# Kernel tuning notes

Measured on AMD Instinct MI355X. Metric: run time of the kernel, lower is better.

## Reference

```python
import jax, jax.numpy as jnp
import numpy as np


def setup_inputs() -> dict:
    key = jax.random.key(0)
    k1, k2, k3, k4 = jax.random.split(key, 4)
    B, T, E, H = 16, 2048, 1024, 128
    x = jax.random.normal(k1, (B, T, E), dtype=jnp.float32)
    Wk = jax.random.normal(k2, (E, H), dtype=jnp.float32) * (E ** -0.5)
    Wq = jax.random.normal(k3, (E, H), dtype=jnp.float32) * (E ** -0.5)
    Wv = jax.random.normal(k4, (E, H), dtype=jnp.float32) * (E ** -0.5)
    return {"x": x, "Wk": Wk, "Wq": Wq, "Wv": Wv}


def reference(x, Wk, Wq, Wv):
    # x: [B,T,E]; Wk/Wq/Wv: [E,H]
    B, T, E = x.shape
    H = Wk.shape[1]
    k = jnp.einsum('bte,eh->bth', x, Wk)
    q = jnp.einsum('bte,eh->bth', x, Wq)
    v = jnp.einsum('bte,eh->bth', x, Wv)
    # scores [B,T,T]; original masks with -inf THEN scales (equivalent math)
    scores = jnp.einsum('bqh,bkh->bqk', q, k) * (H ** -0.5)
    causal = jnp.tril(jnp.ones((T, T), dtype=bool))
    scores = jnp.where(causal, scores, -jnp.inf)
    weights = jax.nn.softmax(scores, axis=-1)
    # dropout disabled (eval mode reference)
    return jnp.einsum('bqk,bkh->bqh', weights, v)
```

## Files before the change

### kernel.cpp

```cpp
#include <hip/hip_runtime.h>

#define B_ 16
#define T_ 2048
#define E_ 1024
#define H_ 128

typedef short bf16x8 __attribute__((ext_vector_type(8)));
typedef float f32x4 __attribute__((ext_vector_type(4)));
typedef unsigned short u16x4 __attribute__((ext_vector_type(4)));

static __device__ __forceinline__ unsigned short f2bf(float f) {
    unsigned int u = __float_as_uint(f);
    u += 0x7FFFu + ((u >> 16) & 1u);
    return (unsigned short)(u >> 16);
}
static __device__ __forceinline__ unsigned int pk2(unsigned short a, unsigned short b) {
    return (unsigned int)a | ((unsigned int)b << 16);
}
static __device__ __forceinline__ bf16x8 frag(uint4 v) {
    return __builtin_bit_cast(bf16x8, v);
}
static __device__ __forceinline__ void gl16(const unsigned short* g, unsigned short* l) {
    __builtin_amdgcn_global_load_lds(
        (const __attribute__((address_space(1))) void*)g,
        (__attribute__((address_space(3))) void*)l, 16, 0, 0);
}

__global__ __launch_bounds__(256) void cvtw_kernel(
    const float* __restrict__ w0, const float* __restrict__ w1,
    const float* __restrict__ w2, unsigned short* __restrict__ wt)
{
    int g   = blockIdx.x * 256 + threadIdx.x;
    int arr = g >> 14;
    int rem = g & 16383;
    int h   = rem >> 7;
    int e0  = (rem & 127) * 8;
    const float* src = (arr == 0) ? w0 : (arr == 1) ? w1 : w2;
    unsigned short b[8];
#pragma unroll
    for (int i = 0; i < 8; i++) b[i] = f2bf(src[(size_t)(e0 + i) * H_ + h]);
    uint4 o;
    o.x = pk2(b[0], b[1]); o.y = pk2(b[2], b[3]);
    o.z = pk2(b[4], b[5]); o.w = pk2(b[6], b[7]);
    *(uint4*)&wt[(size_t)(arr * 128 + h) * E_ + e0] = o;
}

__global__ __launch_bounds__(512, 4) void proj_kernel(
    const float* __restrict__ x,
    const unsigned short* __restrict__ wt,
    unsigned short* __restrict__ q_ws,
    unsigned short* __restrict__ kp_ws,
    unsigned short* __restrict__ vt_ws)
{
    const int m0 = blockIdx.x * 64;
    __shared__ __align__(16) unsigned short As[2][64 * 32];
    __shared__ __align__(16) unsigned short Bs[2][384 * 32];

    const int tid  = threadIdx.x;
    const int lane = tid & 63;
    const int w    = tid >> 6;
    const int quad = lane >> 4;
    const int lm   = lane & 15;
    const int wc   = w * 48;

    const int arow = tid >> 3;
    const int acol = (tid & 7) * 4;
    const float* gx = x + (size_t)(m0 + arow) * E_ + acol;

    const int brow = tid >> 2;
    const int bcol = (tid & 3) * 8;
    const unsigned short* gw = wt + (size_t)brow * E_ + bcol;

    const f32x4 z4 = {0.f, 0.f, 0.f, 0.f};
    f32x4 acc[4][3];
#pragma unroll
    for (int i = 0; i < 4; i++)
#pragma unroll
        for (int j = 0; j < 3; j++) acc[i][j] = z4;

    auto stageB = [&](int kb, int buf) {
        const unsigned short* g = gw + kb * 32;
        unsigned short* l = &Bs[buf][tid * 8];
        gl16(g,                    l);
        gl16(g + (size_t)128 * E_, l + 4096);
        gl16(g + (size_t)256 * E_, l + 8192);
    };
    auto writeA = [&](float4 v, int buf) {
        u16x4 o;
        o[0] = f2bf(v.x); o[1] = f2bf(v.y);
        o[2] = f2bf(v.z); o[3] = f2bf(v.w);
        *(u16x4*)&As[buf][arow * 32 + acol] = o;
    };

    float4 a = *(const float4*)gx;
    stageB(0, 0);
    writeA(a, 0);
    a = *(const float4*)(gx + 32);

    for (int kb = 0; kb < 32; kb++) {
        const int cb = kb & 1;
        __syncthreads();

        const int kb2 = (kb + 2 < 32) ? kb + 2 : 31;
        float4 n = *(const float4*)(gx + kb2 * 32);
        if (kb + 1 < 32) {
            stageB(kb + 1, cb ^ 1);
            writeA(a, cb ^ 1);
        }

        bf16x8 af[4], bf[3];
#pragma unroll
        for (int am = 0; am < 4; am++)
            af[am] = frag(*(const uint4*)&As[cb][(am * 16 + lm) * 32 + quad * 8]);
#pragma unroll
        for (int bn = 0; bn < 3; bn++)
            bf[bn] = frag(*(const uint4*)&Bs[cb][(wc + bn * 16 + lm) * 32 + quad * 8]);
#pragma unroll
        for (int am = 0; am < 4; am++)
#pragma unroll
            for (int bn = 0; bn < 3; bn++)
                acc[am][bn] = __builtin_amdgcn_mfma_f32_16x16x32_bf16(
                    af[am], bf[bn], acc[am][bn], 0, 0, 0);

        a = n;
    }

#pragma unroll
    for (int am = 0; am < 4; am++)
#pragma unroll
        for (int bn = 0; bn < 3; bn++) {
            const int gcol  = wc + bn * 16 + lm;
            const int sel   = gcol >> 7;
            const int c     = gcol & 127;
            const int rbase = m0 + am * 16 + quad * 4;
            const int bb    = rbase >> 11;
            const int t     = rbase & 2047;
            if (sel == 0) {
#pragma unroll
                for (int r = 0; r < 4; r++)
                    q_ws[(size_t)(rbase + r) * H_ + c] = f2bf(acc[am][bn][r]);
            } else if (sel == 1) {
#pragma unroll
                for (int r = 0; r < 4; r++) {
                    int tt = t + r;
                    kp_ws[(size_t)(bb * 64 + (tt >> 5)) * 4096 +
                          (c >> 5) * 1024 + (tt & 31) * 32 + (c & 31)] =
                        f2bf(acc[am][bn][r]);
                }
            } else {
                u16x4 pv;
#pragma unroll
                for (int r = 0; r < 4; r++) pv[r] = f2bf(acc[am][bn][r]);
                *(u16x4*)&vt_ws[((size_t)(bb * 64 + (t >> 5)) * 128 + c) * 32 + (t & 31)] = pv;
            }
        }
}

__global__ __launch_bounds__(256, 2) void attn_kernel(
    const unsigned short* __restrict__ q_ws,
    const unsigned short* __restrict__ kp_ws,
    const unsigned short* __restrict__ vt_ws,
    float* __restrict__ out)
{
    __shared__ __align__(16) unsigned short Ks[3][4096];
    __shared__ __align__(16) unsigned short Vs[3][4096];
    __shared__ __align__(16) unsigned short Ps[4][16][40];

    const int bid   = blockIdx.x;
    const int batch = bid & 15;
    const int p     = (bid >> 4) & 15;
    const int tau   = (bid >> 8) ? (31 - p) : p;
    const int nkt   = 2 * tau + 2;

    const int tid  = threadIdx.x;
    const int lane = tid & 63;
    const int ww   = tid >> 6;
    const int quad = lane >> 4;
    const int lm   = lane & 15;
    const float scale = 0.08838834764831845f;

    bf16x8 ones;
#pragma unroll
    for (int i = 0; i < 8; i++) ones[i] = (short)0x3F80;
    const f32x4 z4 = {0.f, 0.f, 0.f, 0.f};

    const size_t bq = (size_t)batch * T_ * H_;
    const int so = ww * 1024 + lane * 8;
    const unsigned short* Kt = kp_ws + (size_t)(batch * 64) * 4096 + so;
    const unsigned short* Vt = vt_ws + (size_t)(batch * 64) * 4096 + so;

    auto stage = [&](int t, int b) {
        const unsigned short* kg = Kt + (size_t)t * 4096;
        const unsigned short* vg = Vt + (size_t)t * 4096;
        gl16(kg,       &Ks[b][ww * 1024]);
        gl16(kg + 512, &Ks[b][ww * 1024 + 512]);
        gl16(vg,       &Vs[b][ww * 1024]);
        gl16(vg + 512, &Vs[b][ww * 1024 + 512]);
    };

    bf16x8 qf[4];
#pragma unroll
    for (int h = 0; h < 4; h++)
        qf[h] = frag(*(const uint4*)(q_ws + bq +
                 (size_t)(tau * 64 + ww * 16 + lm) * H_ + h * 32 + quad * 8));

    f32x4 o[9];
#pragma unroll
    for (int f = 0; f < 9; f++) o[f] = z4;

    stage(0, 0);
    stage(1, 1);

    for (int kt = 0; kt < nkt; kt++) {
        const int cb = kt % 3;
        asm volatile("s_waitcnt vmcnt(4) lgkmcnt(0)" ::: "memory");
        __builtin_amdgcn_sched_barrier(0);
        __builtin_amdgcn_s_barrier();
        __builtin_amdgcn_sched_barrier(0);

        int ks = kt + 2; if (ks > nkt - 1) ks = nkt - 1;
        stage(ks, (kt + 2) % 3);

        f32x4 st0 = z4, st1 = z4;
        __builtin_amdgcn_s_setprio(1);
#pragma unroll
        for (int h = 0; h < 4; h++) {
            bf16x8 kf0 = frag(*(const uint4*)&Ks[cb][(h * 32 + lm) * 32 + quad * 8]);
            bf16x8 kf1 = frag(*(const uint4*)&Ks[cb][(h * 32 + 16 + lm) * 32 + quad * 8]);
            st0 = __builtin_amdgcn_mfma_f32_16x16x32_bf16(kf0, qf[h], st0, 0, 0, 0);
            st1 = __builtin_amdgcn_mfma_f32_16x16x32_bf16(kf1, qf[h], st1, 0, 0, 0);
        }
        __builtin_amdgcn_s_setprio(0);

        const int qg = tau * 64 + ww * 16 + lm;
        const int k0 = kt * 32;
        u16x4 pa, pb;
#pragma unroll
        for (int r = 0; r < 4; r++) {
            int kv0 = k0 + quad * 4 + r;
            float e0 = __expf(st0[r] * scale);
            float e1 = __expf(st1[r] * scale);
            pa[r] = (kv0      <= qg) ? f2bf(e0) : (unsigned short)0;
            pb[r] = (kv0 + 16 <= qg) ? f2bf(e1) : (unsigned short)0;
        }
        *(u16x4*)&Ps[ww][lm][quad * 4]      = pa;
        *(u16x4*)&Ps[ww][lm][16 + quad * 4] = pb;
        bf16x8 pf = frag(*(const uint4*)&Ps[ww][lm][quad * 8]);

        __builtin_amdgcn_s_setprio(1);
#pragma unroll
        for (int f = 0; f < 8; f++) {
            bf16x8 vfr = frag(*(const uint4*)&Vs[cb][(f * 16 + lm) * 32 + quad * 8]);
            o[f] = __builtin_amdgcn_mfma_f32_16x16x32_bf16(pf, vfr, o[f], 0, 0, 0);
        }
        o[8] = __builtin_amdgcn_mfma_f32_16x16x32_bf16(pf, ones, o[8], 0, 0, 0);
        __builtin_amdgcn_s_setprio(0);
    }

    float* op = out + bq + (size_t)(tau * 64 + ww * 16) * H_;
#pragma unroll
    for (int r = 0; r < 4; r++) {
        float inv = 1.f / o[8][r];
#pragma unroll
        for (int f = 0; f < 8; f++)
            op[(size_t)(quad * 4 + r) * H_ + f * 16 + lm] = o[f][r] * inv;
    }
}

extern "C" void kernel_launch(void* const* d_in, const int* in_sizes, int n_in,
                              void* d_out, int out_size, void* d_ws, size_t ws_size,
                              hipStream_t stream)
{
    const float* x  = (const float*)d_in[0];
    const float* Wk = (const float*)d_in[1];
    const float* Wq = (const float*)d_in[2];
    const float* Wv = (const float*)d_in[3];
    float* out = (float*)d_out;

    const size_t MH = (size_t)B_ * T_ * H_;
    unsigned short* q_ws  = (unsigned short*)d_ws;
    unsigned short* kp_ws = q_ws + MH;
    unsigned short* vt_ws = kp_ws + MH;
    unsigned short* wt    = vt_ws + MH;

    cvtw_kernel<<<dim3(192), dim3(256), 0, stream>>>(Wq, Wk, Wv, wt);
    proj_kernel<<<dim3(512), dim3(512), 0, stream>>>(x, wt, q_ws, kp_ws, vt_ws);
    attn_kernel<<<dim3(512), dim3(256), 0, stream>>>(q_ws, kp_ws, vt_ws, out);
}
```

Before: 283.7 us.

## Retile projection GEMM to 128x128 blocks with a grid split over Q/K/V

```diff
diff --git a/kernel.cpp b/kernel.cpp
--- a/kernel.cpp
+++ b/kernel.cpp
@@ -45,113 +45,125 @@
     *(uint4*)&wt[(size_t)(arr * 128 + h) * E_ + e0] = o;
 }
 
-__global__ __launch_bounds__(512, 4) void proj_kernel(
+__global__ __launch_bounds__(256, 3) void proj_kernel(
     const float* __restrict__ x,
     const unsigned short* __restrict__ wt,
     unsigned short* __restrict__ q_ws,
     unsigned short* __restrict__ kp_ws,
     unsigned short* __restrict__ vt_ws)
 {
-    const int m0 = blockIdx.x * 64;
-    __shared__ __align__(16) unsigned short As[2][64 * 32];
-    __shared__ __align__(16) unsigned short Bs[2][384 * 32];
+    const int m0 = blockIdx.x * 128;
+    const int by = blockIdx.y;
+    __shared__ __align__(16) unsigned short As[2][128 * 32];
+    __shared__ __align__(16) unsigned short Bs[2][128 * 32];
 
     const int tid  = threadIdx.x;
     const int lane = tid & 63;
     const int w    = tid >> 6;
     const int quad = lane >> 4;
     const int lm   = lane & 15;
-    const int wc   = w * 48;
-
-    const int arow = tid >> 3;
-    const int acol = (tid & 7) * 4;
-    const float* gx = x + (size_t)(m0 + arow) * E_ + acol;
-
-    const int brow = tid >> 2;
-    const int bcol = (tid & 3) * 8;
-    const unsigned short* gw = wt + (size_t)brow * E_ + bcol;
+    const int rw   = (w & 1) * 64;
+    const int cw   = (w >> 1) * 64;
+
+    const int srow = w * 32 + (lane >> 2);
+    const int sch  = (lane & 3) * 8;
+    const unsigned short* gb0 = wt + (size_t)(by * 128 + srow) * E_ + sch;
+    const unsigned short* gb1 = gb0 + (size_t)16 * E_;
+
+    const int arow = tid >> 1;
+    const int acs  = (tid & 1) * 16;
+    const float* gxa = x + (size_t)(m0 + arow) * E_ + acs;
 
     const f32x4 z4 = {0.f, 0.f, 0.f, 0.f};
-    f32x4 acc[4][3];
+    f32x4 acc[4][4];
 #pragma unroll
     for (int i = 0; i < 4; i++)
 #pragma unroll
-        for (int j = 0; j < 3; j++) acc[i][j] = z4;
+        for (int j = 0; j < 4; j++) acc[i][j] = z4;
 
     auto stageB = [&](int kb, int buf) {
-        const unsigned short* g = gw + kb * 32;
-        unsigned short* l = &Bs[buf][tid * 8];
-        gl16(g,                    l);
-        gl16(g + (size_t)128 * E_, l + 4096);
-        gl16(g + (size_t)256 * E_, l + 8192);
+        gl16(gb0 + kb * 32, &Bs[buf][w * 1024]);
+        gl16(gb1 + kb * 32, &Bs[buf][w * 1024 + 512]);
     };
-    auto writeA = [&](float4 v, int buf) {
-        u16x4 o;
-        o[0] = f2bf(v.x); o[1] = f2bf(v.y);
-        o[2] = f2bf(v.z); o[3] = f2bf(v.w);
-        *(u16x4*)&As[buf][arow * 32 + acol] = o;
+    float4 av0, av1, av2, av3;
+    auto ldA = [&](int kb) {
+        const float* g = gxa + kb * 32;
+        av0 = *(const float4*)g;
+        av1 = *(const float4*)(g + 4);
+        av2 = *(const float4*)(g + 8);
+        av3 = *(const float4*)(g + 12);
     };
-
-    float4 a = *(const float4*)gx;
+    auto writeA = [&](int buf) {
+        uint4 o0, o1;
+        o0.x = pk2(f2bf(av0.x), f2bf(av0.y));
+        o0.y = pk2(f2bf(av0.z), f2bf(av0.w));
+        o0.z = pk2(f2bf(av1.x), f2bf(av1.y));
+        o0.w = pk2(f2bf(av1.z), f2bf(av1.w));
+        o1.x = pk2(f2bf(av2.x), f2bf(av2.y));
+        o1.y = pk2(f2bf(av2.z), f2bf(av2.w));
+        o1.z = pk2(f2bf(av3.x), f2bf(av3.y));
+        o1.w = pk2(f2bf(av3.z), f2bf(av3.w));
+        *(uint4*)&As[buf][arow * 32 + acs]     = o0;
+        *(uint4*)&As[buf][arow * 32 + acs + 8] = o1;
+    };
+
+    ldA(0);
     stageB(0, 0);
-    writeA(a, 0);
-    a = *(const float4*)(gx + 32);
+    writeA(0);
+    ldA(1);
 
     for (int kb = 0; kb < 32; kb++) {
         const int cb = kb & 1;
         __syncthreads();
 
-        const int kb2 = (kb + 2 < 32) ? kb + 2 : 31;
-        float4 n = *(const float4*)(gx + kb2 * 32);
         if (kb + 1 < 32) {
             stageB(kb + 1, cb ^ 1);
-            writeA(a, cb ^ 1);
-        }
-
-        bf16x8 af[4], bf[3];
+            writeA(cb ^ 1);
+        }
+        ldA((kb + 2 < 32) ? kb + 2 : 31);
+
+        bf16x8 a[4], b[4];
 #pragma unroll
         for (int am = 0; am < 4; am++)
-            af[am] = frag(*(const uint4*)&As[cb][(am * 16 + lm) * 32 + quad * 8]);
-#pragma unroll
-        for (int bn = 0; bn < 3; bn++)
-            bf[bn] = frag(*(const uint4*)&Bs[cb][(wc + bn * 16 + lm) * 32 + quad * 8]);
+            a[am] = frag(*(const uint4*)&As[cb][(rw + am * 16 + lm) * 32 + quad * 8]);
+#pragma unroll
+        for (int bn = 0; bn < 4; bn++)
+            b[bn] = frag(*(const uint4*)&Bs[cb][(cw + bn * 16 + lm) * 32 + quad * 8]);
 #pragma unroll
         for (int am = 0; am < 4; am++)
 #pragma unroll
-            for (int bn = 0; bn < 3; bn++)
+            for (int bn = 0; bn < 4; bn++)
                 acc[am][bn] = __builtin_amdgcn_mfma_f32_16x16x32_bf16(
-                    af[am], bf[bn], acc[am][bn], 0, 0, 0);
-
-        a = n;
+                    a[am], b[bn], acc[am][bn], 0, 0, 0);
     }
 
+    const int bb = m0 >> 11;
+    const int t0 = m0 & 2047;
 #pragma unroll
     for (int am = 0; am < 4; am++)
 #pragma unroll
-        for (int bn = 0; bn < 3; bn++) {
-            const int gcol  = wc + bn * 16 + lm;
-            const int sel   = gcol >> 7;
-            const int c     = gcol & 127;
-            const int rbase = m0 + am * 16 + quad * 4;
-            const int bb    = rbase >> 11;
-            const int t     = rbase & 2047;
-            if (sel == 0) {
+        for (int bn = 0; bn < 4; bn++) {
+            const int col = cw + bn * 16 + lm;
+            if (by == 0) {
+                const int row = m0 + rw + am * 16 + quad * 4;
 #pragma unroll
                 for (int r = 0; r < 4; r++)
-                    q_ws[(size_t)(rbase + r) * H_ + c] = f2bf(acc[am][bn][r]);
-            } else if (sel == 1) {
+                    q_ws[(size_t)(row + r) * H_ + col] = f2bf(acc[am][bn][r]);
+            } else if (by == 1) {
+                const int tl = t0 + rw + am * 16 + quad * 4;
 #pragma unroll
                 for (int r = 0; r < 4; r++) {
-                    int tt = t + r;
-                    kp_ws[(size_t)(bb * 64 + (tt >> 5)) * 4096 +
-                          (c >> 5) * 1024 + (tt & 31) * 32 + (c & 31)] =
+                    int t = tl + r;
+                    kp_ws[(size_t)(bb * 64 + (t >> 5)) * 4096 +
+                          (col >> 5) * 1024 + (t & 31) * 32 + (col & 31)] =
                         f2bf(acc[am][bn][r]);
                 }
             } else {
-                u16x4 pv;
-#pragma unroll
-                for (int r = 0; r < 4; r++) pv[r] = f2bf(acc[am][bn][r]);
-                *(u16x4*)&vt_ws[((size_t)(bb * 64 + (t >> 5)) * 128 + c) * 32 + (t & 31)] = pv;
+                const int tt = t0 + rw + am * 16 + quad * 4;
+                u16x4 p;
+#pragma unroll
+                for (int r = 0; r < 4; r++) p[r] = f2bf(acc[am][bn][r]);
+                *(u16x4*)&vt_ws[((size_t)(bb * 64 + (tt >> 5)) * 128 + col) * 32 + (tt & 31)] = p;
             }
         }
 }
@@ -284,6 +296,6 @@
     unsigned short* wt    = vt_ws + MH;
 
     cvtw_kernel<<<dim3(192), dim3(256), 0, stream>>>(Wq, Wk, Wv, wt);
-    proj_kernel<<<dim3(512), dim3(512), 0, stream>>>(x, wt, q_ws, kp_ws, vt_ws);
+    proj_kernel<<<dim3(256, 3), dim3(256), 0, stream>>>(x, wt, q_ws, kp_ws, vt_ws);
     attn_kernel<<<dim3(512), dim3(256), 0, stream>>>(q_ws, kp_ws, vt_ws, out);
 }
```

New measurement: 418.7 us. +47.6%, slower.

## Split projection output columns across two blocks with 256-thread blocks

Applied to the files above, without the earlier changes.

```diff
diff --git a/kernel.cpp b/kernel.cpp
--- a/kernel.cpp
+++ b/kernel.cpp
@@ -45,7 +45,7 @@
     *(uint4*)&wt[(size_t)(arr * 128 + h) * E_ + e0] = o;
 }
 
-__global__ __launch_bounds__(512, 4) void proj_kernel(
+__global__ __launch_bounds__(256, 4) void proj_kernel(
     const float* __restrict__ x,
     const unsigned short* __restrict__ wt,
     unsigned short* __restrict__ q_ws,
@@ -53,8 +53,9 @@
     unsigned short* __restrict__ vt_ws)
 {
     const int m0 = blockIdx.x * 64;
+    const int c0 = blockIdx.y * 192;
     __shared__ __align__(16) unsigned short As[2][64 * 32];
-    __shared__ __align__(16) unsigned short Bs[2][384 * 32];
+    __shared__ __align__(16) unsigned short Bs[2][192 * 32];
 
     const int tid  = threadIdx.x;
     const int lane = tid & 63;
@@ -63,13 +64,11 @@
     const int lm   = lane & 15;
     const int wc   = w * 48;
 
-    const int arow = tid >> 3;
-    const int acol = (tid & 7) * 4;
+    const int arow = tid >> 2;
+    const int acol = (tid & 3) * 8;
     const float* gx = x + (size_t)(m0 + arow) * E_ + acol;
 
-    const int brow = tid >> 2;
-    const int bcol = (tid & 3) * 8;
-    const unsigned short* gw = wt + (size_t)brow * E_ + bcol;
+    const unsigned short* gw = wt + (size_t)(c0 + (tid >> 2)) * E_ + (tid & 3) * 8;
 
     const f32x4 z4 = {0.f, 0.f, 0.f, 0.f};
     f32x4 acc[4][3];
@@ -82,30 +81,35 @@
         const unsigned short* g = gw + kb * 32;
         unsigned short* l = &Bs[buf][tid * 8];
         gl16(g,                    l);
+        gl16(g + (size_t)64  * E_, l + 2048);
         gl16(g + (size_t)128 * E_, l + 4096);
-        gl16(g + (size_t)256 * E_, l + 8192);
     };
-    auto writeA = [&](float4 v, int buf) {
-        u16x4 o;
-        o[0] = f2bf(v.x); o[1] = f2bf(v.y);
-        o[2] = f2bf(v.z); o[3] = f2bf(v.w);
-        *(u16x4*)&As[buf][arow * 32 + acol] = o;
+    auto writeA = [&](float4 v0, float4 v1, int buf) {
+        uint4 o;
+        o.x = pk2(f2bf(v0.x), f2bf(v0.y));
+        o.y = pk2(f2bf(v0.z), f2bf(v0.w));
+        o.z = pk2(f2bf(v1.x), f2bf(v1.y));
+        o.w = pk2(f2bf(v1.z), f2bf(v1.w));
+        *(uint4*)&As[buf][arow * 32 + acol] = o;
     };
 
-    float4 a = *(const float4*)gx;
+    float4 a0 = *(const float4*)gx;
+    float4 a1 = *(const float4*)(gx + 4);
     stageB(0, 0);
-    writeA(a, 0);
-    a = *(const float4*)(gx + 32);
+    writeA(a0, a1, 0);
+    a0 = *(const float4*)(gx + 32);
+    a1 = *(const float4*)(gx + 36);
 
     for (int kb = 0; kb < 32; kb++) {
         const int cb = kb & 1;
         __syncthreads();
 
         const int kb2 = (kb + 2 < 32) ? kb + 2 : 31;
-        float4 n = *(const float4*)(gx + kb2 * 32);
+        float4 n0 = *(const float4*)(gx + kb2 * 32);
+        float4 n1 = *(const float4*)(gx + kb2 * 32 + 4);
         if (kb + 1 < 32) {
             stageB(kb + 1, cb ^ 1);
-            writeA(a, cb ^ 1);
+            writeA(a0, a1, cb ^ 1);
         }
 
         bf16x8 af[4], bf[3];
@@ -122,14 +126,14 @@
                 acc[am][bn] = __builtin_amdgcn_mfma_f32_16x16x32_bf16(
                     af[am], bf[bn], acc[am][bn], 0, 0, 0);
 
-        a = n;
+        a0 = n0; a1 = n1;
     }
 
 #pragma unroll
     for (int am = 0; am < 4; am++)
 #pragma unroll
         for (int bn = 0; bn < 3; bn++) {
-            const int gcol  = wc + bn * 16 + lm;
+            const int gcol  = c0 + wc + bn * 16 + lm;
             const int sel   = gcol >> 7;
             const int c     = gcol & 127;
             const int rbase = m0 + am * 16 + quad * 4;
@@ -284,6 +288,6 @@
     unsigned short* wt    = vt_ws + MH;
 
     cvtw_kernel<<<dim3(192), dim3(256), 0, stream>>>(Wq, Wk, Wv, wt);
-    proj_kernel<<<dim3(512), dim3(512), 0, stream>>>(x, wt, q_ws, kp_ws, vt_ws);
+    proj_kernel<<<dim3(512, 2), dim3(256), 0, stream>>>(x, wt, q_ws, kp_ws, vt_ws);
     attn_kernel<<<dim3(512), dim3(256), 0, stream>>>(q_ws, kp_ws, vt_ws, out);
 }
```

New measurement: 292.4 us. 3.1% more time.
